# Kernel optimization log

Hardware: AMD Instinct MI355X
Metric: run time of the kernel (lower is better)

The kernel has to match this reference:

```python
import jax, jax.numpy as jnp
import numpy as np

B, N, D = 8, 512, 1024
E, H, TOP_K = 8, 8, 2
HD = D // H
EPS = 1e-5


def setup_inputs() -> dict:
    key = jax.random.key(0)
    ks = jax.random.split(key, 8)
    # kaiming_uniform with a=sqrt(5) over fan_in=N -> bound = sqrt(6/((1+5)*N)) = 1/sqrt(N)
    bound_w = 1.0 / np.sqrt(N)
    bound_lin = 1.0 / np.sqrt(D)
    return {
        "x": jax.random.normal(ks[0], (B, N, D), dtype=jnp.float32),
        "weight": jax.random.uniform(ks[1], (E, H, N, N), jnp.float32, -bound_w, bound_w),
        "bias": jnp.zeros((E, H, N), jnp.float32),
        "router_w": jax.random.uniform(ks[2], (E, D), jnp.float32, -bound_lin, bound_lin),
        "in_w": jax.random.uniform(ks[3], (D, D), jnp.float32, -bound_lin, bound_lin),
        "in_b": jax.random.uniform(ks[4], (D,), jnp.float32, -bound_lin, bound_lin),
        "out_w": jax.random.uniform(ks[5], (D, D), jnp.float32, -bound_lin, bound_lin),
        "out_b": jax.random.uniform(ks[6], (D,), jnp.float32, -bound_lin, bound_lin),
    }


def reference(x, weight, bias, router_w, in_w, in_b, out_w, out_b):
    # Router: mean-pool tokens, linear, softmax, top-k
    router_logits = x.mean(axis=1) @ router_w.T              # (B, E)
    router_probs = jax.nn.softmax(router_logits, axis=-1)
    top_w, top_i = jax.lax.top_k(router_probs, TOP_K)        # (B, K)
    top_w = top_w / top_w.sum(axis=-1, keepdims=True)

    # Input projection -> (B, H, hd, N), layer-norm over token axis N (no affine)
    xp = x @ in_w.T + in_b                                   # (B, N, D)
    xr = xp.reshape(B, N, H, HD).transpose(0, 2, 3, 1)       # (B, H, hd, N)
    mu = xr.mean(axis=-1, keepdims=True)
    var = xr.var(axis=-1, keepdims=True)
    xn = (xr - mu) * jax.lax.rsqrt(var + EPS)

    # Gather per-(batch, head, k) NxN expert matrices, row-softmax
    w = weight[top_i].transpose(0, 2, 1, 3, 4)               # (B, H, K, N, N)
    b = bias[top_i].transpose(0, 2, 1, 3)                    # (B, H, K, N)
    w_attn = jax.nn.softmax(w, axis=-1)

    # out[b,h,k,d,m] = sum_n xn[b,h,d,n] * w_attn[b,h,k,m,n]
    out = jnp.einsum('bhdn,bhkmn->bhkdm', xn, w_attn)
    out = out + b[:, :, :, None, :]                          # (B, H, K, hd, N)
    out = (out * top_w[:, None, :, None, None]).sum(axis=2)  # (B, H, hd, N)

    out = out.transpose(0, 3, 1, 2).reshape(B, N, D)         # (B, N, D)
    out = out @ out_w.T + out_b

    # Load-balancing aux loss
    top1 = top_i[:, 0]
    expert_mask = jax.nn.one_hot(top1, E, dtype=jnp.float32)
    aux = E * (router_probs.mean(axis=0) * expert_mask.mean(axis=0)).sum()
    return out, aux
```

## Files before the change

### kernel.cpp

```cpp
#include <hip/hip_runtime.h>
#include <hip/hip_bf16.h>

#define Bv 8
#define Nv 512
#define Dv 1024
#define Ev 8
#define Hv 8
#define HDv 128
#define EPSv 1e-5f

typedef __attribute__((ext_vector_type(8))) short short8;
typedef __attribute__((ext_vector_type(4))) float f32x4;

__device__ __forceinline__ unsigned short f2b(float f) {
    __hip_bfloat16 h = __float2bfloat16(f);
    return *reinterpret_cast<unsigned short*>(&h);
}
__device__ __forceinline__ float bf2f(unsigned int u) {
    union { unsigned int i; float f; } v; v.i = u << 16; return v.f;
}

__device__ __forceinline__ void gld16(const void* g, void* l) {
    __builtin_amdgcn_global_load_lds(
        (const __attribute__((address_space(1))) void*)(uintptr_t)(g),
        (__attribute__((address_space(3))) void*)(uintptr_t)(l), 16, 0, 0);
}

__global__ __launch_bounds__(256) void k_preA(const float* __restrict__ x,
                                              const float* __restrict__ w1,
                                              const float* __restrict__ w2,
                                              unsigned short* __restrict__ xb,
                                              float* __restrict__ part_x,
                                              unsigned short* __restrict__ w1b,
                                              unsigned short* __restrict__ w2b) {
    int bid = blockIdx.x;
    int t = threadIdx.x;
    if (bid < 128) {
        int b = bid >> 4, c = bid & 15;
        const float* px = x + ((size_t)b * Nv + c * 32) * Dv + t * 4;
        unsigned short* qx = xb + ((size_t)b * Nv + c * 32) * Dv + t * 4;
        float4 s4 = make_float4(0.f, 0.f, 0.f, 0.f);
        #pragma unroll 8
        for (int r = 0; r < 32; ++r) {
            float4 v = *(const float4*)(px + (size_t)r * Dv);
            s4.x += v.x; s4.y += v.y; s4.z += v.z; s4.w += v.w;
            uint2 pk;
            pk.x = (unsigned)f2b(v.x) | ((unsigned)f2b(v.y) << 16);
            pk.y = (unsigned)f2b(v.z) | ((unsigned)f2b(v.w) << 16);
            *(uint2*)(qx + (size_t)r * Dv) = pk;
        }
        *(float4*)(part_x + ((size_t)(b * 16 + c)) * Dv + t * 4) = s4;
        return;
    }
    const float* src; unsigned short* dst; int base;
    if (bid < 256) { src = w1; dst = w1b; base = (bid - 128) * 8192; }
    else           { src = w2; dst = w2b; base = (bid - 256) * 8192; }
    #pragma unroll
    for (int i = 0; i < 8; ++i) {
        float4 a = *(const float4*)(src + base + i * 1024 + t * 4);
        uint2 p;
        p.x = (unsigned)f2b(a.x) | ((unsigned)f2b(a.y) << 16);
        p.y = (unsigned)f2b(a.z) | ((unsigned)f2b(a.w) << 16);
        *(uint2*)(dst + base + i * 1024 + t * 4) = p;
    }
}

template <int MODE>
__global__ __launch_bounds__(256) void k_gemm(
    const unsigned short* __restrict__ A,
    const unsigned short* __restrict__ W,
    const float* __restrict__ bias,
    void* __restrict__ Cv,
    float2* __restrict__ part,
    const float* __restrict__ part_x,
    float* __restrict__ xmean,
    int M, int Nn, int K) {
    __shared__ __align__(16) unsigned short sA[3][128 * 64];
    __shared__ __align__(16) unsigned short sB[3][128 * 64];
    const int t = threadIdx.x;
    const int bn = blockIdx.x * 128;
    const int bm = blockIdx.y * 128;
    const int lane = t & 63;
    const int w = t >> 6, wm = w >> 1, wn = w & 1;
    const int fr = lane & 15, fq = lane >> 4;
    const int NT = K >> 6;
    f32x4 acc[4][4] = {};

#define STAGE(s, k0)                                                        \
    {                                                                       \
        _Pragma("unroll")                                                   \
        for (int i_ = 0; i_ < 4; ++i_) {                                    \
            int c_ = t + i_ * 256;                                          \
            int row_ = c_ >> 3, col_ = c_ & 7;                              \
            int cs_ = col_ ^ (row_ & 7);                                    \
            gld16(A + (size_t)(bm + row_) * K + (k0) + cs_ * 8, &sA[s][c_ * 8]); \
            gld16(W + (size_t)(bn + row_) * K + (k0) + cs_ * 8, &sB[s][c_ * 8]); \
        }                                                                   \
    }

    STAGE(0, 0);
    STAGE(1, 64);
    if (MODE == 2) {
        int blk = blockIdx.y * 8 + blockIdx.x;
        int o = blk * 32 + (t >> 3);
        int c2 = t & 7;
        int b2 = o >> 10, d2 = o & 1023;
        float S = part_x[((size_t)(b2 * 16 + c2)) * Dv + d2]
                + part_x[((size_t)(b2 * 16 + c2 + 8)) * Dv + d2];
        S += __shfl_xor(S, 1); S += __shfl_xor(S, 2); S += __shfl_xor(S, 4);
        if (c2 == 0) xmean[o] = S * (1.f / Nv);
    }
    for (int it = 0; it < NT; ++it) {
        if (it + 2 < NT) {
            STAGE((it + 2) % 3, (it + 2) * 64);
            asm volatile("s_waitcnt vmcnt(16)" ::: "memory");
        } else if (it + 1 < NT) {
            asm volatile("s_waitcnt vmcnt(8)" ::: "memory");
        } else {
            asm volatile("s_waitcnt vmcnt(0)" ::: "memory");
        }
        __builtin_amdgcn_s_barrier();
        const unsigned short* pA = sA[it % 3];
        const unsigned short* pB = sB[it % 3];
        #pragma unroll
        for (int kk = 0; kk < 2; ++kk) {
            short8 af[4], bv[4];
            #pragma unroll
            for (int i = 0; i < 4; ++i)
                af[i] = *(const short8*)&pA[(wm * 64 + i * 16 + fr) * 64 + (((kk << 2) + fq) ^ (fr & 7)) * 8];
            #pragma unroll
            for (int j = 0; j < 4; ++j)
                bv[j] = *(const short8*)&pB[(wn * 64 + j * 16 + fr) * 64 + (((kk << 2) + fq) ^ (fr & 7)) * 8];
            #pragma unroll
            for (int i = 0; i < 4; ++i)
                #pragma unroll
                for (int j = 0; j < 4; ++j)
                    acc[i][j] = __builtin_amdgcn_mfma_f32_16x16x32_bf16(af[i], bv[j], acc[i][j], 0, 0, 0);
        }
        __builtin_amdgcn_s_barrier();
    }
#undef STAGE
    if (MODE == 0) {
        #pragma unroll
        for (int j = 0; j < 4; ++j) {
            const int n = bn + wn * 64 + j * 16 + fr;
            const float bj = bias[n];
            #pragma unroll
            for (int i = 0; i < 4; ++i) {
                const int m0 = bm + wm * 64 + i * 16 + fq * 4;
                #pragma unroll
                for (int r = 0; r < 4; ++r)
                    ((float*)Cv)[(size_t)(m0 + r) * Nn + n] = acc[i][j][r] + bj;
            }
        }
    } else {
        unsigned short* sc = &sA[0][0];
        float2* red = (float2*)&sB[0][0];
        const int bB   = bm >> 9;
        const int tok0 = bm & 511;
        const int chunk = (bm >> 7) & 3;
        #pragma unroll
        for (int j = 0; j < 4; ++j) {
            const int col = wn * 64 + j * 16 + fr;
            const float bj = bias[bn + col];
            float s = 0.f, q = 0.f;
            #pragma unroll
            for (int i = 0; i < 4; ++i) {
                const int row0 = wm * 64 + i * 16 + fq * 4;
                #pragma unroll
                for (int r = 0; r < 4; r += 2) {
                    float v0 = acc[i][j][r] + bj;
                    float v1 = acc[i][j][r + 1] + bj;
                    s += v0 + v1;
                    q = fmaf(v0, v0, fmaf(v1, v1, q));
                    unsigned int pk = (unsigned int)f2b(v0) | ((unsigned int)f2b(v1) << 16);
                    *(unsigned int*)&sc[col * 136 + row0 + r] = pk;
                }
            }
            red[col * 8 + wm * 4 + fq] = make_float2(s, q);
        }
        __syncthreads();
        if (t < 128) {
            float S = 0.f, Q = 0.f;
            #pragma unroll
            for (int k = 0; k < 8; ++k) { float2 v = red[t * 8 + k]; S += v.x; Q += v.y; }
            part[((size_t)bB * Dv + bn + t) * 4 + chunk] = make_float2(S, Q);
        }
        unsigned short* dst = (unsigned short*)Cv;
        #pragma unroll
        for (int k = 0; k < 8; ++k) {
            const int c = t + k * 256;
            const int dl = c >> 4, tk = c & 15;
            uint4 v = *(const uint4*)&sc[dl * 136 + tk * 8];
            *(uint4*)&dst[((size_t)bB * Dv + bn + dl) * Nv + tok0 + tk * 8] = v;
        }
    }
}

__global__ __launch_bounds__(256) void k_mixg(
    const float* __restrict__ weight,
    const unsigned short* __restrict__ xpT,
    const float* __restrict__ bias,
    const float* __restrict__ xmean,
    const float* __restrict__ router_w,
    const float2* __restrict__ part,
    unsigned short* __restrict__ y,
    float* __restrict__ aux_out) {
    __shared__ __align__(16) unsigned short sA0[2][128 * 64];
    __shared__ __align__(16) unsigned short sA1[2][128 * 64];
    __shared__ __align__(16) unsigned short sB[2][128 * 64];
    __shared__ float rowc0[128], rowc1[128];
    __shared__ float probs[Bv][Ev];
    __shared__ float twsh[Bv][2];
    __shared__ int   tsel[Bv][2];
    __shared__ int   top1s[Bv];
    const int t = threadIdx.x;
    const int bm = blockIdx.x * 128;
    const int bh = blockIdx.y;
    const int b = bh >> 3, h = bh & 7;

    {
        int pid = t >> 2, l = t & 3;
        int rb = pid >> 3, re = pid & 7;
        const float4* xm = (const float4*)(xmean + rb * Dv);
        const float4* rw = (const float4*)(router_w + re * Dv);
        float s = 0.f;
        #pragma unroll
        for (int j = 0; j < 64; ++j) {
            float4 aa = xm[l + j * 4], ww = rw[l + j * 4];
            s = fmaf(aa.x, ww.x, s); s = fmaf(aa.y, ww.y, s);
            s = fmaf(aa.z, ww.z, s); s = fmaf(aa.w, ww.w, s);
        }
        s += __shfl_xor(s, 1); s += __shfl_xor(s, 2);
        if (l == 0) probs[rb][re] = s;
    }
    __syncthreads();
    if (t < Bv) {
        int bb = t;
        float mx = -1e30f;
        for (int e2 = 0; e2 < Ev; ++e2) mx = fmaxf(mx, probs[bb][e2]);
        float sum = 0.f;
        for (int e2 = 0; e2 < Ev; ++e2) { float v = __expf(probs[bb][e2] - mx); probs[bb][e2] = v; sum += v; }
        float inv = 1.f / sum;
        for (int e2 = 0; e2 < Ev; ++e2) probs[bb][e2] *= inv;
        int i0 = 0; float p0 = probs[bb][0];
        for (int e2 = 1; e2 < Ev; ++e2) if (probs[bb][e2] > p0) { p0 = probs[bb][e2]; i0 = e2; }
        int i1 = -1; float p1 = -1.f;
        for (int e2 = 0; e2 < Ev; ++e2) if (e2 != i0 && probs[bb][e2] > p1) { p1 = probs[bb][e2]; i1 = e2; }
        float s2 = p0 + p1;
        tsel[bb][0] = i0; tsel[bb][1] = i1;
        twsh[bb][0] = p0 / s2; twsh[bb][1] = p1 / s2;
        top1s[bb] = i0;
    }
    __syncthreads();
    if (blockIdx.x == 0 && bh == 0 && t == 0) {
        float aux = 0.f;
        for (int e2 = 0; e2 < Ev; ++e2) {
            float pm = 0.f, mm = 0.f;
            for (int bb = 0; bb < Bv; ++bb) { pm += probs[bb][e2]; mm += (top1s[bb] == e2) ? 1.f : 0.f; }
            aux += (pm / Bv) * (mm / Bv);
        }
        *aux_out = aux * Ev;
    }
    const int e0 = tsel[b][0], e1 = tsel[b][1];
    const float tw0 = twsh[b][0], tw1 = twsh[b][1];

    const int lane = t & 63;
    const int w = t >> 6, wm = w >> 1, wn = w & 1;
    const int fr = lane & 15, fq = lane >> 4;

    float rstd_j[4], nmr_j[4];
    #pragma unroll
    for (int j = 0; j < 4; ++j) {
        const int dg = h * HDv + wn * 64 + j * 16 + fr;
        const float2* pp = part + ((size_t)b * Dv + dg) * 4;
        float S = 0.f, Q = 0.f;
        #pragma unroll
        for (int cc = 0; cc < 4; ++cc) { float2 v = pp[cc]; S += v.x; Q += v.y; }
        float mu = S * (1.f / Nv);
        float var = Q * (1.f / Nv) - mu * mu;
        float rs = rsqrtf(var + EPSv);
        rstd_j[j] = rs; nmr_j[j] = -mu * rs;
    }

    const float* W0 = weight + (size_t)(e0 * Hv + h) * Nv * Nv;
    const float* W1 = weight + (size_t)(e1 * Hv + h) * Nv * Nv;
    const unsigned short* Bb = xpT + ((size_t)b * Dv + h * HDv) * Nv;

    const int NT = Nv >> 6;
    f32x4 acc0[4][4] = {}, acc1[4][4] = {};
    float4 ra0[4][2], ra1[4][2];
    float s0p[4] = {0.f, 0.f, 0.f, 0.f}, s1p[4] = {0.f, 0.f, 0.f, 0.f};

#define BSTAGE(s, k0)                                                       \
    {                                                                       \
        _Pragma("unroll")                                                   \
        for (int i_ = 0; i_ < 4; ++i_) {                                    \
            int c_ = t + i_ * 256;                                          \
            int row_ = c_ >> 3, col_ = c_ & 7;                              \
            int cs_ = col_ ^ (row_ & 7);                                    \
            gld16(Bb + (size_t)row_ * Nv + (k0) + cs_ * 8, &sB[s][c_ * 8]); \
        }                                                                   \
    }
#define ALOAD(k0)                                                           \
    {                                                                       \
        _Pragma("unroll")                                                   \
        for (int i_ = 0; i_ < 4; ++i_) {                                    \
            int c_ = t + i_ * 256;                                          \
            int row_ = c_ >> 3, col_ = c_ & 7;                              \
            int cs_ = col_ ^ (row_ & 7);                                    \
            size_t off_ = (size_t)(bm + row_) * Nv + (k0) + cs_ * 8;        \
            ra0[i_][0] = *(const float4*)&W0[off_];                         \
            ra0[i_][1] = *(const float4*)&W0[off_ + 4];                     \
            ra1[i_][0] = *(const float4*)&W1[off_];                         \
            ra1[i_][1] = *(const float4*)&W1[off_ + 4];                     \
        }                                                                   \
    }

    BSTAGE(0, 0);
    ALOAD(0);
    for (int it = 0; it < NT; ++it) {
        if (it + 1 < NT) {
            BSTAGE((it + 1) & 1, (it + 1) * 64);
            asm volatile("s_waitcnt vmcnt(4)" ::: "memory");
        } else {
            asm volatile("s_waitcnt vmcnt(0)" ::: "memory");
        }
        #pragma unroll
        for (int i = 0; i < 4; ++i) {
            int c = t + i * 256;
            float e0v[8], e1v[8];
            const float4 a0 = ra0[i][0], a1 = ra0[i][1];
            const float4 b0 = ra1[i][0], b1 = ra1[i][1];
            e0v[0] = __expf(a0.x); e0v[1] = __expf(a0.y);
            e0v[2] = __expf(a0.z); e0v[3] = __expf(a0.w);
            e0v[4] = __expf(a1.x); e0v[5] = __expf(a1.y);
            e0v[6] = __expf(a1.z); e0v[7] = __expf(a1.w);
            e1v[0] = __expf(b0.x); e1v[1] = __expf(b0.y);
            e1v[2] = __expf(b0.z); e1v[3] = __expf(b0.w);
            e1v[4] = __expf(b1.x); e1v[5] = __expf(b1.y);
            e1v[6] = __expf(b1.z); e1v[7] = __expf(b1.w);
            s0p[i] += ((e0v[0] + e0v[1]) + (e0v[2] + e0v[3]))
                    + ((e0v[4] + e0v[5]) + (e0v[6] + e0v[7]));
            s1p[i] += ((e1v[0] + e1v[1]) + (e1v[2] + e1v[3]))
                    + ((e1v[4] + e1v[5]) + (e1v[6] + e1v[7]));
            uint4 p0, p1;
            p0.x = (unsigned)f2b(e0v[0]) | ((unsigned)f2b(e0v[1]) << 16);
            p0.y = (unsigned)f2b(e0v[2]) | ((unsigned)f2b(e0v[3]) << 16);
            p0.z = (unsigned)f2b(e0v[4]) | ((unsigned)f2b(e0v[5]) << 16);
            p0.w = (unsigned)f2b(e0v[6]) | ((unsigned)f2b(e0v[7]) << 16);
            p1.x = (unsigned)f2b(e1v[0]) | ((unsigned)f2b(e1v[1]) << 16);
            p1.y = (unsigned)f2b(e1v[2]) | ((unsigned)f2b(e1v[3]) << 16);
            p1.z = (unsigned)f2b(e1v[4]) | ((unsigned)f2b(e1v[5]) << 16);
            p1.w = (unsigned)f2b(e1v[6]) | ((unsigned)f2b(e1v[7]) << 16);
            *(uint4*)&sA0[it & 1][c * 8] = p0;
            *(uint4*)&sA1[it & 1][c * 8] = p1;
        }
        if (it + 1 < NT) ALOAD((it + 1) * 64);
        asm volatile("s_waitcnt lgkmcnt(0)" ::: "memory");
        __builtin_amdgcn_s_barrier();
        const unsigned short* pA0 = sA0[it & 1];
        const unsigned short* pA1 = sA1[it & 1];
        const unsigned short* pB = sB[it & 1];
        #pragma unroll
        for (int kk = 0; kk < 2; ++kk) {
            short8 bv[4];
            #pragma unroll
            for (int j = 0; j < 4; ++j)
                bv[j] = *(const short8*)&pB[(wn * 64 + j * 16 + fr) * 64 + (((kk << 2) + fq) ^ (fr & 7)) * 8];
            #pragma unroll
            for (int i = 0; i < 4; ++i) {
                const int aoff = (wm * 64 + i * 16 + fr) * 64 + (((kk << 2) + fq) ^ (fr & 7)) * 8;
                short8 af0 = *(const short8*)&pA0[aoff];
                short8 af1 = *(const short8*)&pA1[aoff];
                #pragma unroll
                for (int j = 0; j < 4; ++j)
                    acc0[i][j] = __builtin_amdgcn_mfma_f32_16x16x32_bf16(af0, bv[j], acc0[i][j], 0, 0, 0);
                #pragma unroll
                for (int j = 0; j < 4; ++j)
                    acc1[i][j] = __builtin_amdgcn_mfma_f32_16x16x32_bf16(af1, bv[j], acc1[i][j], 0, 0, 0);
            }
        }
        __builtin_amdgcn_s_barrier();
    }
#undef BSTAGE
#undef ALOAD

    #pragma unroll
    for (int i = 0; i < 4; ++i) {
        #pragma unroll
        for (int off = 1; off < 8; off <<= 1) {
            s0p[i] += __shfl_xor(s0p[i], off);
            s1p[i] += __shfl_xor(s1p[i], off);
        }
        int row = (t >> 3) + i * 32;
        if ((t & 7) == 0) {
            rowc0[row] = tw0 / s0p[i];
            rowc1[row] = tw1 / s1p[i];
        }
    }
    __syncthreads();

    #pragma unroll
    for (int i = 0; i < 4; ++i) {
        #pragma unroll
        for (int r = 0; r < 4; ++r) {
            const int ml = wm * 64 + i * 16 + fq * 4 + r;
            const int m = bm + ml;
            const float c0m = rowc0[ml], c1m = rowc1[ml];
            const float br = tw0 * bias[(size_t)(e0 * Hv + h) * Nv + m]
                           + tw1 * bias[(size_t)(e1 * Hv + h) * Nv + m];
            #pragma unroll
            for (int j = 0; j < 4; ++j) {
                const int d = wn * 64 + j * 16 + fr;
                float vb = c0m * acc0[i][j][r] + c1m * acc1[i][j][r];
                float v = fmaf(vb, rstd_j[j], nmr_j[j] + br);
                y[((size_t)b * Nv + m) * Dv + h * HDv + d] = f2b(v);
            }
        }
    }
}

extern "C" void kernel_launch(void* const* d_in, const int* in_sizes, int n_in,
                              void* d_out, int out_size, void* d_ws, size_t ws_size,
                              hipStream_t stream) {
    const float* x        = (const float*)d_in[0];
    const float* weight   = (const float*)d_in[1];
    const float* bias     = (const float*)d_in[2];
    const float* router_w = (const float*)d_in[3];
    const float* in_w     = (const float*)d_in[4];
    const float* in_b     = (const float*)d_in[5];
    const float* out_w    = (const float*)d_in[6];
    const float* out_b    = (const float*)d_in[7];
    float* out = (float*)d_out;

    if (ws_size < ((size_t)63 << 20)) return;

    char* wsb = (char*)d_ws;
    float*  xmean  = (float*)(wsb);
    float2* part   = (float2*)(wsb + (64 << 10));
    float*  part_x = (float*)(wsb + (512 << 10));
    unsigned short* in_wb  = (unsigned short*)(wsb + ((size_t)2 << 20));
    unsigned short* out_wb = (unsigned short*)(wsb + ((size_t)4 << 20));
    unsigned short* xb     = (unsigned short*)(wsb + ((size_t)8 << 20));
    unsigned short* xpT    = (unsigned short*)(wsb + ((size_t)16 << 20));
    unsigned short* y = xb;

    k_preA<<<384, 256, 0, stream>>>(x, in_w, out_w, xb, part_x, in_wb, out_wb);
    k_gemm<2><<<dim3(8, 32), 256, 0, stream>>>(xb, in_wb, in_b, xpT, part, part_x, xmean,
                                               Bv * Nv, Dv, Dv);
    k_mixg<<<dim3(4, 64), 256, 0, stream>>>(weight, xpT, bias, xmean, router_w, part, y,
                                            out + (size_t)Bv * Nv * Dv);
    k_gemm<0><<<dim3(8, 32), 256, 0, stream>>>(y, out_wb, out_b, out, nullptr, nullptr, nullptr,
                                               Bv * Nv, Dv, Dv);
}
```

Measured before the change: 73.86 us.

## Halve mixing-kernel row tile and prefetch expert weights two stages ahead

The expert-mixing kernel now handles 64 output rows per block instead of 128, which doubles the grid to 512 blocks so more compute units have work. The loop is fully unrolled with two alternating register sets, so fp32 expert weights are loaded two k-steps ahead. The A-operand LDS buffers become single-buffered to save shared memory. In exchange, each block re-reads the full xpT operand tile and recomputes the router prologue, so redundant traffic and setup work double.

```diff
diff --git a/kernel.cpp b/kernel.cpp
--- a/kernel.cpp
+++ b/kernel.cpp
@@ -206,16 +206,16 @@
     const float2* __restrict__ part,
     unsigned short* __restrict__ y,
     float* __restrict__ aux_out) {
-    __shared__ __align__(16) unsigned short sA0[2][128 * 64];
-    __shared__ __align__(16) unsigned short sA1[2][128 * 64];
+    __shared__ __align__(16) unsigned short sA0[64 * 64];
+    __shared__ __align__(16) unsigned short sA1[64 * 64];
     __shared__ __align__(16) unsigned short sB[2][128 * 64];
-    __shared__ float rowc0[128], rowc1[128];
+    __shared__ float rowc0[64], rowc1[64];
     __shared__ float probs[Bv][Ev];
     __shared__ float twsh[Bv][2];
     __shared__ int   tsel[Bv][2];
     __shared__ int   top1s[Bv];
     const int t = threadIdx.x;
-    const int bm = blockIdx.x * 128;
+    const int bm = blockIdx.x * 64;
     const int bh = blockIdx.y;
     const int b = bh >> 3, h = bh & 7;
 
@@ -287,10 +287,9 @@
     const float* W1 = weight + (size_t)(e1 * Hv + h) * Nv * Nv;
     const unsigned short* Bb = xpT + ((size_t)b * Dv + h * HDv) * Nv;
 
-    const int NT = Nv >> 6;
-    f32x4 acc0[4][4] = {}, acc1[4][4] = {};
-    float4 ra0[4][2], ra1[4][2];
-    float s0p[4] = {0.f, 0.f, 0.f, 0.f}, s1p[4] = {0.f, 0.f, 0.f, 0.f};
+    f32x4 acc0[2][4] = {}, acc1[2][4] = {};
+    float4 raA0[2][2], raA1[2][2], raB0[2][2], raB1[2][2];
+    float s0p[2] = {0.f, 0.f}, s1p[2] = {0.f, 0.f};
 
 #define BSTAGE(s, k0)                                                       \
     {                                                                       \
@@ -302,92 +301,108 @@
             gld16(Bb + (size_t)row_ * Nv + (k0) + cs_ * 8, &sB[s][c_ * 8]); \
         }                                                                   \
     }
-#define ALOAD(k0)                                                           \
+#define ALOADG(RA0, RA1, k0)                                                \
     {                                                                       \
         _Pragma("unroll")                                                   \
-        for (int i_ = 0; i_ < 4; ++i_) {                                    \
+        for (int i_ = 0; i_ < 2; ++i_) {                                    \
             int c_ = t + i_ * 256;                                          \
             int row_ = c_ >> 3, col_ = c_ & 7;                              \
             int cs_ = col_ ^ (row_ & 7);                                    \
             size_t off_ = (size_t)(bm + row_) * Nv + (k0) + cs_ * 8;        \
-            ra0[i_][0] = *(const float4*)&W0[off_];                         \
-            ra0[i_][1] = *(const float4*)&W0[off_ + 4];                     \
-            ra1[i_][0] = *(const float4*)&W1[off_];                         \
-            ra1[i_][1] = *(const float4*)&W1[off_ + 4];                     \
+            RA0[i_][0] = *(const float4*)&W0[off_];                         \
+            RA0[i_][1] = *(const float4*)&W0[off_ + 4];                     \
+            RA1[i_][0] = *(const float4*)&W1[off_];                         \
+            RA1[i_][1] = *(const float4*)&W1[off_ + 4];                     \
         }                                                                   \
     }
+#define BLEND(RA0, RA1)                                                     \
+    {                                                                       \
+        _Pragma("unroll")                                                   \
+        for (int i_ = 0; i_ < 2; ++i_) {                                    \
+            int c_ = t + i_ * 256;                                          \
+            float e0v[8], e1v[8];                                           \
+            const float4 a0_ = RA0[i_][0], a1_ = RA0[i_][1];                \
+            const float4 b0_ = RA1[i_][0], b1_ = RA1[i_][1];                \
+            e0v[0] = __expf(a0_.x); e0v[1] = __expf(a0_.y);                 \
+            e0v[2] = __expf(a0_.z); e0v[3] = __expf(a0_.w);                 \
+            e0v[4] = __expf(a1_.x); e0v[5] = __expf(a1_.y);                 \
+            e0v[6] = __expf(a1_.z); e0v[7] = __expf(a1_.w);                 \
+            e1v[0] = __expf(b0_.x); e1v[1] = __expf(b0_.y);                 \
+            e1v[2] = __expf(b0_.z); e1v[3] = __expf(b0_.w);                 \
+            e1v[4] = __expf(b1_.x); e1v[5] = __expf(b1_.y);                 \
+            e1v[6] = __expf(b1_.z); e1v[7] = __expf(b1_.w);                 \
+            s0p[i_] += ((e0v[0] + e0v[1]) + (e0v[2] + e0v[3]))              \
+                     + ((e0v[4] + e0v[5]) + (e0v[6] + e0v[7]));             \
+            s1p[i_] += ((e1v[0] + e1v[1]) + (e1v[2] + e1v[3]))              \
+                     + ((e1v[4] + e1v[5]) + (e1v[6] + e1v[7]));             \
+            uint4 p0_, p1_;                                                 \
+            p0_.x = (unsigned)f2b(e0v[0]) | ((unsigned)f2b(e0v[1]) << 16);  \
+            p0_.y = (unsigned)f2b(e0v[2]) | ((unsigned)f2b(e0v[3]) << 16);  \
+            p0_.z = (unsigned)f2b(e0v[4]) | ((unsigned)f2b(e0v[5]) << 16);  \
+            p0_.w = (unsigned)f2b(e0v[6]) | ((unsigned)f2b(e0v[7]) << 16);  \
+            p1_.x = (unsigned)f2b(e1v[0]) | ((unsigned)f2b(e1v[1]) << 16);  \
+            p1_.y = (unsigned)f2b(e1v[2]) | ((unsigned)f2b(e1v[3]) << 16);  \
+            p1_.z = (unsigned)f2b(e1v[4]) | ((unsigned)f2b(e1v[5]) << 16);  \
+            p1_.w = (unsigned)f2b(e1v[6]) | ((unsigned)f2b(e1v[7]) << 16);  \
+            *(uint4*)&sA0[c_ * 8] = p0_;                                    \
+            *(uint4*)&sA1[c_ * 8] = p1_;                                    \
+        }                                                                   \
+    }
+#define MFMAPH(sbuf)                                                        \
+    {                                                                       \
+        const unsigned short* pB = sB[sbuf];                                \
+        _Pragma("unroll")                                                   \
+        for (int kk = 0; kk < 2; ++kk) {                                    \
+            short8 bv[4];                                                   \
+            _Pragma("unroll")                                               \
+            for (int j = 0; j < 4; ++j)                                     \
+                bv[j] = *(const short8*)&pB[(wn * 64 + j * 16 + fr) * 64 + (((kk << 2) + fq) ^ (fr & 7)) * 8]; \
+            _Pragma("unroll")                                               \
+            for (int i = 0; i < 2; ++i) {                                   \
+                const int aoff = (wm * 32 + i * 16 + fr) * 64 + (((kk << 2) + fq) ^ (fr & 7)) * 8; \
+                short8 af0 = *(const short8*)&sA0[aoff];                    \
+                short8 af1 = *(const short8*)&sA1[aoff];                    \
+                _Pragma("unroll")                                           \
+                for (int j = 0; j < 4; ++j)                                 \
+                    acc0[i][j] = __builtin_amdgcn_mfma_f32_16x16x32_bf16(af0, bv[j], acc0[i][j], 0, 0, 0); \
+                _Pragma("unroll")                                           \
+                for (int j = 0; j < 4; ++j)                                 \
+                    acc1[i][j] = __builtin_amdgcn_mfma_f32_16x16x32_bf16(af1, bv[j], acc1[i][j], 0, 0, 0); \
+            }                                                               \
+        }                                                                   \
+    }
+#define FITER(it, RA0, RA1)                                                 \
+    {                                                                       \
+        if ((it) + 1 < 8) BSTAGE(((it) + 1) & 1, ((it) + 1) * 64);          \
+        if ((it) < 7) { asm volatile("s_waitcnt vmcnt(12)" ::: "memory"); } \
+        else          { asm volatile("s_waitcnt vmcnt(0)" ::: "memory"); }  \
+        BLEND(RA0, RA1);                                                    \
+        if ((it) + 2 < 8) ALOADG(RA0, RA1, ((it) + 2) * 64);                \
+        asm volatile("s_waitcnt lgkmcnt(0)" ::: "memory");                  \
+        __builtin_amdgcn_s_barrier();                                       \
+        MFMAPH((it) & 1);                                                   \
+        __builtin_amdgcn_s_barrier();                                       \
+    }
 
     BSTAGE(0, 0);
-    ALOAD(0);
-    for (int it = 0; it < NT; ++it) {
-        if (it + 1 < NT) {
-            BSTAGE((it + 1) & 1, (it + 1) * 64);
-            asm volatile("s_waitcnt vmcnt(4)" ::: "memory");
-        } else {
-            asm volatile("s_waitcnt vmcnt(0)" ::: "memory");
-        }
-        #pragma unroll
-        for (int i = 0; i < 4; ++i) {
-            int c = t + i * 256;
-            float e0v[8], e1v[8];
-            const float4 a0 = ra0[i][0], a1 = ra0[i][1];
-            const float4 b0 = ra1[i][0], b1 = ra1[i][1];
-            e0v[0] = __expf(a0.x); e0v[1] = __expf(a0.y);
-            e0v[2] = __expf(a0.z); e0v[3] = __expf(a0.w);
-            e0v[4] = __expf(a1.x); e0v[5] = __expf(a1.y);
-            e0v[6] = __expf(a1.z); e0v[7] = __expf(a1.w);
-            e1v[0] = __expf(b0.x); e1v[1] = __expf(b0.y);
-            e1v[2] = __expf(b0.z); e1v[3] = __expf(b0.w);
-            e1v[4] = __expf(b1.x); e1v[5] = __expf(b1.y);
-            e1v[6] = __expf(b1.z); e1v[7] = __expf(b1.w);
-            s0p[i] += ((e0v[0] + e0v[1]) + (e0v[2] + e0v[3]))
-                    + ((e0v[4] + e0v[5]) + (e0v[6] + e0v[7]));
-            s1p[i] += ((e1v[0] + e1v[1]) + (e1v[2] + e1v[3]))
-                    + ((e1v[4] + e1v[5]) + (e1v[6] + e1v[7]));
-            uint4 p0, p1;
-            p0.x = (unsigned)f2b(e0v[0]) | ((unsigned)f2b(e0v[1]) << 16);
-            p0.y = (unsigned)f2b(e0v[2]) | ((unsigned)f2b(e0v[3]) << 16);
-            p0.z = (unsigned)f2b(e0v[4]) | ((unsigned)f2b(e0v[5]) << 16);
-            p0.w = (unsigned)f2b(e0v[6]) | ((unsigned)f2b(e0v[7]) << 16);
-            p1.x = (unsigned)f2b(e1v[0]) | ((unsigned)f2b(e1v[1]) << 16);
-            p1.y = (unsigned)f2b(e1v[2]) | ((unsigned)f2b(e1v[3]) << 16);
-            p1.z = (unsigned)f2b(e1v[4]) | ((unsigned)f2b(e1v[5]) << 16);
-            p1.w = (unsigned)f2b(e1v[6]) | ((unsigned)f2b(e1v[7]) << 16);
-            *(uint4*)&sA0[it & 1][c * 8] = p0;
-            *(uint4*)&sA1[it & 1][c * 8] = p1;
-        }
-        if (it + 1 < NT) ALOAD((it + 1) * 64);
-        asm volatile("s_waitcnt lgkmcnt(0)" ::: "memory");
-        __builtin_amdgcn_s_barrier();
-        const unsigned short* pA0 = sA0[it & 1];
-        const unsigned short* pA1 = sA1[it & 1];
-        const unsigned short* pB = sB[it & 1];
-        #pragma unroll
-        for (int kk = 0; kk < 2; ++kk) {
-            short8 bv[4];
-            #pragma unroll
-            for (int j = 0; j < 4; ++j)
-                bv[j] = *(const short8*)&pB[(wn * 64 + j * 16 + fr) * 64 + (((kk << 2) + fq) ^ (fr & 7)) * 8];
-            #pragma unroll
-            for (int i = 0; i < 4; ++i) {
-                const int aoff = (wm * 64 + i * 16 + fr) * 64 + (((kk << 2) + fq) ^ (fr & 7)) * 8;
-                short8 af0 = *(const short8*)&pA0[aoff];
-                short8 af1 = *(const short8*)&pA1[aoff];
-                #pragma unroll
-                for (int j = 0; j < 4; ++j)
-                    acc0[i][j] = __builtin_amdgcn_mfma_f32_16x16x32_bf16(af0, bv[j], acc0[i][j], 0, 0, 0);
-                #pragma unroll
-                for (int j = 0; j < 4; ++j)
-                    acc1[i][j] = __builtin_amdgcn_mfma_f32_16x16x32_bf16(af1, bv[j], acc1[i][j], 0, 0, 0);
-            }
-        }
-        __builtin_amdgcn_s_barrier();
-    }
+    ALOADG(raA0, raA1, 0);
+    ALOADG(raB0, raB1, 64);
+    FITER(0, raA0, raA1);
+    FITER(1, raB0, raB1);
+    FITER(2, raA0, raA1);
+    FITER(3, raB0, raB1);
+    FITER(4, raA0, raA1);
+    FITER(5, raB0, raB1);
+    FITER(6, raA0, raA1);
+    FITER(7, raB0, raB1);
 #undef BSTAGE
-#undef ALOAD
+#undef ALOADG
+#undef BLEND
+#undef MFMAPH
+#undef FITER
 
     #pragma unroll
-    for (int i = 0; i < 4; ++i) {
+    for (int i = 0; i < 2; ++i) {
         #pragma unroll
         for (int off = 1; off < 8; off <<= 1) {
             s0p[i] += __shfl_xor(s0p[i], off);
@@ -402,10 +417,10 @@
     __syncthreads();
 
     #pragma unroll
-    for (int i = 0; i < 4; ++i) {
+    for (int i = 0; i < 2; ++i) {
         #pragma unroll
         for (int r = 0; r < 4; ++r) {
-            const int ml = wm * 64 + i * 16 + fq * 4 + r;
+            const int ml = wm * 32 + i * 16 + fq * 4 + r;
             const int m = bm + ml;
             const float c0m = rowc0[ml], c1m = rowc1[ml];
             const float br = tw0 * bias[(size_t)(e0 * Hv + h) * Nv + m]
@@ -449,7 +464,7 @@
     k_preA<<<384, 256, 0, stream>>>(x, in_w, out_w, xb, part_x, in_wb, out_wb);
     k_gemm<2><<<dim3(8, 32), 256, 0, stream>>>(xb, in_wb, in_b, xpT, part, part_x, xmean,
                                                Bv * Nv, Dv, Dv);
-    k_mixg<<<dim3(4, 64), 256, 0, stream>>>(weight, xpT, bias, xmean, router_w, part, y,
+    k_mixg<<<dim3(8, 64), 256, 0, stream>>>(weight, xpT, bias, xmean, router_w, part, y,
                                             out + (size_t)Bv * Nv * Dv);
     k_gemm<0><<<dim3(8, 32), 256, 0, stream>>>(y, out_wb, out_b, out, nullptr, nullptr, nullptr,
                                                Bv * Nv, Dv, Dv);
```

Result: slower. 82.98 us (+12.4%).
